# Optimization experiments

Measured on AMD Instinct MI355X. Metric: run time of the kernel, lower is better.

Reference implementation:

```python
import jax, jax.numpy as jnp
import numpy as np

H = 16  # n_heads

def setup_inputs() -> dict:
    key = jax.random.key(0)
    ks = jax.random.split(key, 8)
    B, S, D = 2, 2048, 1024
    q = jax.random.normal(ks[0], (B, S, D), dtype=jnp.float32)
    k = jax.random.normal(ks[1], (B, S, D), dtype=jnp.float32)
    v = jax.random.normal(ks[2], (B, S, D), dtype=jnp.float32)
    mask = jnp.ones((B, S, S), dtype=jnp.int32)
    scale = 1.0 / np.sqrt(D)
    Wq = jax.random.normal(ks[3], (D, D), dtype=jnp.float32) * scale
    Wk = jax.random.normal(ks[4], (D, D), dtype=jnp.float32) * scale
    Wv = jax.random.normal(ks[5], (D, D), dtype=jnp.float32) * scale
    Wo = jax.random.normal(ks[6], (D, D), dtype=jnp.float32) * scale
    return {"q": q, "k": k, "v": v, "mask": mask,
            "Wq": Wq, "Wk": Wk, "Wv": Wv, "Wo": Wo}

def reference(q, k, v, mask, Wq, Wk, Wv, Wo):
    B, S, D = q.shape
    dk = D // H
    # nn.Linear(bias=False): y = x @ W.T
    query = (q @ Wq.T).reshape(B, S, H, dk).transpose(0, 2, 1, 3)  # [B,H,S,dk]
    key_  = (k @ Wk.T).reshape(B, S, H, dk).transpose(0, 2, 1, 3)
    value = (v @ Wv.T).reshape(B, S, H, dk).transpose(0, 2, 1, 3)
    scores = jnp.einsum('bhqd,bhkd->bhqk', query, key_) / jnp.sqrt(jnp.float32(dk))
    scores = jnp.where(mask[:, None, :, :] == 0, jnp.float32(-1e9), scores)
    attn = jax.nn.softmax(scores, axis=-1)  # dropout=0.0 -> identity
    x = jnp.einsum('bhqk,bhkd->bhqd', attn, value)  # [B,H,S,dk]
    x = x.transpose(0, 2, 1, 3).reshape(B, S, D)
    return x @ Wo.T
```

## Files before the change

kernel.cpp:

```cpp
#include <hip/hip_runtime.h>
#include <hip/hip_bf16.h>

#define B_ 2
#define S_ 2048
#define D_ 1024
#define H_ 16

typedef __bf16 bf16x8 __attribute__((ext_vector_type(8)));
typedef __bf16 bf16x4v __attribute__((ext_vector_type(4)));
typedef float f32x4 __attribute__((ext_vector_type(4)));

__device__ __forceinline__ float exp2fast(float x) {
  return __builtin_amdgcn_exp2f(x);
}

__device__ __forceinline__ unsigned short f2bf(float f) {
  unsigned int u = __float_as_uint(f);
  u += 0x7fff + ((u >> 16) & 1);
  return (unsigned short)(u >> 16);
}

__device__ __forceinline__ void gload_lds16(const void* g, void* l) {
  __builtin_amdgcn_global_load_lds(
      (const __attribute__((address_space(1))) void*)g,
      (__attribute__((address_space(3))) void*)l, 16, 0, 0);
}

__global__ __launch_bounds__(256) void cvt_qkv(
    const float* __restrict__ a, const float* __restrict__ b, const float* __restrict__ c,
    unsigned short* __restrict__ da, unsigned short* __restrict__ db,
    unsigned short* __restrict__ dc, int n4) {
  const int z = blockIdx.z;
  const float* s = z == 0 ? a : (z == 1 ? b : c);
  unsigned short* d = z == 0 ? da : (z == 1 ? db : dc);
  int stride = gridDim.x * blockDim.x;
  for (int i = blockIdx.x * blockDim.x + threadIdx.x; i < n4; i += stride) {
    float4 f = ((const float4*)s)[i];
    ushort4 o;
    o.x = f2bf(f.x); o.y = f2bf(f.y); o.z = f2bf(f.z); o.w = f2bf(f.w);
    ((ushort4*)d)[i] = o;
  }
}

__global__ __launch_bounds__(256) void cvt_w(
    const float* __restrict__ a, const float* __restrict__ b,
    const float* __restrict__ c, const float* __restrict__ d,
    unsigned short* __restrict__ da, unsigned short* __restrict__ db,
    unsigned short* __restrict__ dc, unsigned short* __restrict__ dd, int n4) {
  const int z = blockIdx.z;
  const float* s = z == 0 ? a : (z == 1 ? b : (z == 2 ? c : d));
  unsigned short* o = z == 0 ? da : (z == 1 ? db : (z == 2 ? dc : dd));
  int stride = gridDim.x * blockDim.x;
  for (int i = blockIdx.x * blockDim.x + threadIdx.x; i < n4; i += stride) {
    float4 f = ((const float4*)s)[i];
    ushort4 u;
    u.x = f2bf(f.x); u.y = f2bf(f.y); u.z = f2bf(f.z); u.w = f2bf(f.w);
    ((ushort4*)o)[i] = u;
  }
}

__global__ __launch_bounds__(256) void mask_check(const int* __restrict__ m,
                                                  int* __restrict__ flag, int n4) {
  int stride = gridDim.x * blockDim.x;
  bool z = false;
  for (int i = blockIdx.x * blockDim.x + threadIdx.x; i < n4; i += stride) {
    int4 v = ((const int4*)m)[i];
    z |= (v.x == 0) || (v.y == 0) || (v.z == 0) || (v.w == 0);
  }
  if (__any(z)) {
    if ((threadIdx.x & 63) == 0) atomicOr(flag, 1);
  }
}

__device__ __forceinline__ void gemm_core(
    const unsigned short* __restrict__ A, const unsigned short* __restrict__ W,
    unsigned short* As, unsigned short* Bs, int rowBase, int colBase,
    f32x4 (&acc)[4][4]) {
  const int tid = threadIdx.x, lane = tid & 63, w = tid >> 6;
  const int wm = w >> 1, wn = w & 1, l15 = lane & 15, l4 = lane >> 4;
  for (int kt = 0; kt < 16; ++kt) {
#pragma unroll
    for (int i = 0; i < 4; i++) {
      int chunk = (w * 4 + i) * 64 + lane;
      int row = chunk >> 3, c = chunk & 7;
      int cs = c ^ (row & 7);
      gload_lds16(A + (size_t)(rowBase + row) * 1024 + kt * 64 + cs * 8,
                  (char*)As + (w * 4 + i) * 1024);
      gload_lds16(W + (size_t)(colBase + row) * 1024 + kt * 64 + cs * 8,
                  (char*)Bs + (w * 4 + i) * 1024);
    }
    __syncthreads();
#pragma unroll
    for (int ks = 0; ks < 2; ks++) {
      bf16x8 af[4], bfr[4];
#pragma unroll
      for (int mi = 0; mi < 4; mi++) {
        int row = wm * 64 + mi * 16 + l15;
        af[mi] = *(const bf16x8*)((const char*)As + row * 128 +
                                  (((ks * 4 + l4) ^ (row & 7)) << 4));
      }
#pragma unroll
      for (int ni = 0; ni < 4; ni++) {
        int row = wn * 64 + ni * 16 + l15;
        bfr[ni] = *(const bf16x8*)((const char*)Bs + row * 128 +
                                   (((ks * 4 + l4) ^ (row & 7)) << 4));
      }
#pragma unroll
      for (int mi = 0; mi < 4; mi++)
#pragma unroll
        for (int ni = 0; ni < 4; ni++)
          acc[mi][ni] = __builtin_amdgcn_mfma_f32_16x16x32_bf16(
              af[mi], bfr[ni], acc[mi][ni], 0, 0, 0);
    }
    __syncthreads();
  }
}

__global__ __launch_bounds__(256, 2) void gemm_qkv(
    const unsigned short* __restrict__ qA, const unsigned short* __restrict__ kA,
    const unsigned short* __restrict__ vA,
    const unsigned short* __restrict__ Wq, const unsigned short* __restrict__ Wk,
    const unsigned short* __restrict__ Wv,
    unsigned short* __restrict__ Qp, unsigned short* __restrict__ Kp,
    unsigned short* __restrict__ Vtp) {
  __shared__ unsigned short As[128 * 64], Bs[128 * 64];
  const int z = blockIdx.z;
  const unsigned short* A = z == 0 ? qA : (z == 1 ? kA : vA);
  const unsigned short* W = z == 0 ? Wq : (z == 1 ? Wk : Wv);
  const int rowBase = blockIdx.y * 128, colBase = blockIdx.x * 128;
  f32x4 acc[4][4] = {};
  gemm_core(A, W, As, Bs, rowBase, colBase, acc);
  const int tid = threadIdx.x, lane = tid & 63, w = tid >> 6;
  const int wm = w >> 1, wn = w & 1, l15 = lane & 15, l4 = lane >> 4;
#pragma unroll
  for (int mi = 0; mi < 4; mi++)
#pragma unroll
    for (int ni = 0; ni < 4; ni++)
#pragma unroll
      for (int r = 0; r < 4; r++) {
        int gr = rowBase + wm * 64 + mi * 16 + l4 * 4 + r;
        int gc = colBase + wn * 64 + ni * 16 + l15;
        int b = gr >> 11, s = gr & 2047, h = gc >> 6, d = gc & 63;
        float v = acc[mi][ni][r];
        if (z == 0)
          Qp[(((size_t)(b * 16 + h) * 2048 + s) << 6) + d] =
              f2bf(v * 0.18033688011112042f);
        else if (z == 1)
          Kp[(((size_t)(b * 16 + h) * 2048 + s) << 6) + d] = f2bf(v);
        else
          Vtp[((size_t)(b * 16 + h) * 64 + d) * 2048 + s] = f2bf(v);
      }
}

__global__ __launch_bounds__(256, 2) void gemm_o(
    const unsigned short* __restrict__ A, const unsigned short* __restrict__ W,
    float* __restrict__ Out) {
  __shared__ unsigned short As[128 * 64], Bs[128 * 64];
  const int rowBase = blockIdx.y * 128, colBase = blockIdx.x * 128;
  f32x4 acc[4][4] = {};
  gemm_core(A, W, As, Bs, rowBase, colBase, acc);
  const int tid = threadIdx.x, lane = tid & 63, w = tid >> 6;
  const int wm = w >> 1, wn = w & 1, l15 = lane & 15, l4 = lane >> 4;
#pragma unroll
  for (int mi = 0; mi < 4; mi++)
#pragma unroll
    for (int ni = 0; ni < 4; ni++)
#pragma unroll
      for (int r = 0; r < 4; r++) {
        int gr = rowBase + wm * 64 + mi * 16 + l4 * 4 + r;
        int gc = colBase + wn * 64 + ni * 16 + l15;
        Out[(size_t)gr * 1024 + gc] = acc[mi][ni][r];
      }
}

__global__ __launch_bounds__(256, 2) void attn(
    const unsigned short* __restrict__ Qp, const unsigned short* __restrict__ Kp,
    const unsigned short* __restrict__ Vt, unsigned short* __restrict__ Xo,
    const int* __restrict__ flag, const int* __restrict__ mask) {
  __shared__ unsigned short Ks[2][64 * 64];
  __shared__ unsigned short Vs[2][64 * 64];
  __shared__ unsigned short Pl[4][32][72];
  const int tid = threadIdx.x, lane = tid & 63, w = tid >> 6;
  const int l15 = lane & 15, l4 = lane >> 4;
  const int h = blockIdx.y, b = blockIdx.z;
  const int bh = b * H_ + h;
  const int q0 = blockIdx.x * 128 + w * 32;
  const int hz = *flag;

  bf16x8 qf[2][2];
#pragma unroll
  for (int qg = 0; qg < 2; qg++)
#pragma unroll
    for (int ks = 0; ks < 2; ks++)
      qf[qg][ks] = *(const bf16x8*)(Qp + ((size_t)bh * S_ + q0 + qg * 16 + l15) * 64 +
                                    ks * 32 + l4 * 8);

  float m[2] = {-__builtin_inff(), -__builtin_inff()};
  float l[2] = {0.f, 0.f};
  f32x4 accOT[2][4] = {};

  auto stage = [&](int kt, int buf) {
#pragma unroll
    for (int i = 0; i < 2; i++) {
      int ch = (w * 2 + i) * 64 + lane;
      int row = ch >> 3, c = ch & 7;
      int cs = c ^ (row & 7);
      gload_lds16(Kp + ((size_t)bh * S_ + kt * 64 + row) * 64 + cs * 8,
                  (char*)&Ks[buf][0] + (w * 2 + i) * 1024);
      gload_lds16(Vt + ((size_t)bh * 64 + row) * S_ + kt * 64 + cs * 8,
                  (char*)&Vs[buf][0] + (w * 2 + i) * 1024);
    }
  };

  stage(0, 0);
  __syncthreads();

  for (int kt = 0; kt < 32; ++kt) {
    const int cur = kt & 1;
    if (kt < 31) stage(kt + 1, cur ^ 1);

    f32x4 s[2][4] = {};
#pragma unroll
    for (int ks = 0; ks < 2; ks++) {
      bf16x8 kf[4];
#pragma unroll
      for (int kb = 0; kb < 4; kb++) {
        int row = kb * 16 + l15;
        kf[kb] = *(const bf16x8*)((const char*)&Ks[cur][0] + row * 128 +
                                  (((ks * 4 + l4) ^ (row & 7)) << 4));
      }
#pragma unroll
      for (int qg = 0; qg < 2; qg++)
#pragma unroll
        for (int kb = 0; kb < 4; kb++)
          s[qg][kb] = __builtin_amdgcn_mfma_f32_16x16x32_bf16(kf[kb], qf[qg][ks],
                                                              s[qg][kb], 0, 0, 0);
    }

    if (hz) {
#pragma unroll
      for (int qg = 0; qg < 2; qg++)
#pragma unroll
        for (int kb = 0; kb < 4; kb++)
#pragma unroll
          for (int r = 0; r < 4; r++) {
            int kc = kt * 64 + kb * 16 + l4 * 4 + r;
            if (mask[((size_t)b * S_ + q0 + qg * 16 + l15) * S_ + kc] == 0)
              s[qg][kb][r] = -1e9f;
          }
    }

    float mx[2];
#pragma unroll
    for (int qg = 0; qg < 2; qg++) {
      float m0 = fmaxf(fmaxf(s[qg][0][0], s[qg][0][1]), fmaxf(s[qg][0][2], s[qg][0][3]));
      float m1 = fmaxf(fmaxf(s[qg][1][0], s[qg][1][1]), fmaxf(s[qg][1][2], s[qg][1][3]));
      float m2 = fmaxf(fmaxf(s[qg][2][0], s[qg][2][1]), fmaxf(s[qg][2][2], s[qg][2][3]));
      float m3 = fmaxf(fmaxf(s[qg][3][0], s[qg][3][1]), fmaxf(s[qg][3][2], s[qg][3][3]));
      float v = fmaxf(fmaxf(m0, m1), fmaxf(m2, m3));
      v = fmaxf(v, __shfl_xor(v, 16));
      v = fmaxf(v, __shfl_xor(v, 32));
      mx[qg] = v;
    }

    if (!__all(mx[0] - m[0] <= 8.f && mx[1] - m[1] <= 8.f)) {
#pragma unroll
      for (int qg = 0; qg < 2; qg++) {
        float mn = fmaxf(m[qg], mx[qg]);
        float al = exp2fast(m[qg] - mn);
        m[qg] = mn;
        l[qg] *= al;
#pragma unroll
        for (int db = 0; db < 4; db++) accOT[qg][db] *= al;
      }
    }

#pragma unroll
    for (int qg = 0; qg < 2; qg++) {
      float rs = 0.f;
#pragma unroll
      for (int kb = 0; kb < 4; kb++) {
        bf16x4v pk;
#pragma unroll
        for (int r = 0; r < 4; r++) {
          float p = exp2fast(s[qg][kb][r] - m[qg]);
          rs += p;
          pk[r] = (__bf16)p;
        }
        *(bf16x4v*)(&Pl[w][qg * 16 + l15][kb * 16 + l4 * 4]) = pk;
      }
      rs += __shfl_xor(rs, 16);
      rs += __shfl_xor(rs, 32);
      l[qg] += rs;
    }

#pragma unroll
    for (int ks = 0; ks < 2; ks++) {
      bf16x8 vf[4], pa[2];
#pragma unroll
      for (int qg = 0; qg < 2; qg++)
        pa[qg] = *(const bf16x8*)((const char*)&Pl[w][qg * 16 + l15][0] +
                                  ks * 64 + l4 * 16);
#pragma unroll
      for (int db = 0; db < 4; db++) {
        int row = db * 16 + l15;
        vf[db] = *(const bf16x8*)((const char*)&Vs[cur][0] + row * 128 +
                                  (((ks * 4 + l4) ^ (row & 7)) << 4));
      }
#pragma unroll
      for (int qg = 0; qg < 2; qg++)
#pragma unroll
        for (int db = 0; db < 4; db++)
          accOT[qg][db] = __builtin_amdgcn_mfma_f32_16x16x32_bf16(vf[db], pa[qg],
                                                                  accOT[qg][db], 0, 0, 0);
    }
    __syncthreads();
  }

#pragma unroll
  for (int qg = 0; qg < 2; qg++) {
    float rl = 1.0f / l[qg];
    const int q = q0 + qg * 16 + l15;
#pragma unroll
    for (int db = 0; db < 4; db++) {
      bf16x4v o;
#pragma unroll
      for (int r = 0; r < 4; r++) o[r] = (__bf16)(accOT[qg][db][r] * rl);
      *(bf16x4v*)(Xo + (((size_t)(b * S_ + q)) << 10) + h * 64 + db * 16 + l4 * 4) = o;
    }
  }
}

extern "C" void kernel_launch(void* const* d_in, const int* in_sizes, int n_in,
                              void* d_out, int out_size, void* d_ws, size_t ws_size,
                              hipStream_t stream) {
  const float* q = (const float*)d_in[0];
  const float* k = (const float*)d_in[1];
  const float* v = (const float*)d_in[2];
  const int* mask = (const int*)d_in[3];
  const float* Wq = (const float*)d_in[4];
  const float* Wk = (const float*)d_in[5];
  const float* Wv = (const float*)d_in[6];
  const float* Wo = (const float*)d_in[7];

  char* ws = (char*)d_ws;
  const size_t MB = 1024 * 1024;
  unsigned short* qb16 = (unsigned short*)(ws);
  unsigned short* kb16 = (unsigned short*)(ws + 8 * MB);
  unsigned short* vb16 = (unsigned short*)(ws + 16 * MB);
  unsigned short* Wq16 = (unsigned short*)(ws + 24 * MB);
  unsigned short* Wk16 = (unsigned short*)(ws + 26 * MB);
  unsigned short* Wv16 = (unsigned short*)(ws + 28 * MB);
  unsigned short* Wo16 = (unsigned short*)(ws + 30 * MB);
  unsigned short* Qp = (unsigned short*)(ws + 32 * MB);
  unsigned short* Kp = (unsigned short*)(ws + 40 * MB);
  unsigned short* Vtp = (unsigned short*)(ws + 48 * MB);
  int* flag = (int*)(ws + 56 * MB);
  unsigned short* Xo = qb16;

  (void)hipMemsetAsync(flag, 0, 4, stream);
  cvt_qkv<<<dim3(1024, 1, 3), 256, 0, stream>>>(q, k, v, qb16, kb16, vb16,
                                                (B_ * S_ * D_) / 4);
  cvt_w<<<dim3(256, 1, 4), 256, 0, stream>>>(Wq, Wk, Wv, Wo, Wq16, Wk16, Wv16, Wo16,
                                             (D_ * D_) / 4);
  mask_check<<<dim3(2048), 256, 0, stream>>>(mask, flag, (B_ * S_ * S_) / 4);
  gemm_qkv<<<dim3(8, 32, 3), 256, 0, stream>>>(qb16, kb16, vb16, Wq16, Wk16, Wv16,
                                               Qp, Kp, Vtp);
  attn<<<dim3(16, 16, 2), 256, 0, stream>>>(Qp, Kp, Vtp, Xo, flag, mask);
  gemm_o<<<dim3(8, 32), 256, 0, stream>>>(Xo, Wo16, (float*)d_out);
}
```

Before: 158.3 us.

## Fuse prep kernels and load attention K/V directly into registers

The three conversion and mask-check kernels are merged into one prep launch, which removes launch overhead and lets the launches overlap. The attention kernel drops its LDS staging and block-wide barriers for K and V: each wave loads K and V fragments straight from global memory into registers, with K double-buffered in registers. The attention grid is also remapped so blocks that share a head are spread across the grid. In exchange, every wave re-reads the same K/V tiles from global memory or L2, and register pressure goes up.

New measurement: 208.0 us. 1.31x slower.

```diff
diff --git a/kernel.cpp b/kernel.cpp
--- a/kernel.cpp
+++ b/kernel.cpp
@@ -26,49 +26,53 @@
       (__attribute__((address_space(3))) void*)l, 16, 0, 0);
 }
 
-__global__ __launch_bounds__(256) void cvt_qkv(
-    const float* __restrict__ a, const float* __restrict__ b, const float* __restrict__ c,
-    unsigned short* __restrict__ da, unsigned short* __restrict__ db,
-    unsigned short* __restrict__ dc, int n4) {
+__global__ __launch_bounds__(256) void prep(
+    const float* __restrict__ q, const float* __restrict__ k,
+    const float* __restrict__ v, const int* __restrict__ mask,
+    const float* __restrict__ Wq, const float* __restrict__ Wk,
+    const float* __restrict__ Wv, const float* __restrict__ Wo,
+    unsigned short* __restrict__ qb, unsigned short* __restrict__ kb,
+    unsigned short* __restrict__ vb,
+    unsigned short* __restrict__ Wqb, unsigned short* __restrict__ Wkb,
+    unsigned short* __restrict__ Wvb, unsigned short* __restrict__ Wob,
+    int* __restrict__ flag) {
   const int z = blockIdx.z;
-  const float* s = z == 0 ? a : (z == 1 ? b : c);
-  unsigned short* d = z == 0 ? da : (z == 1 ? db : dc);
-  int stride = gridDim.x * blockDim.x;
-  for (int i = blockIdx.x * blockDim.x + threadIdx.x; i < n4; i += stride) {
-    float4 f = ((const float4*)s)[i];
-    ushort4 o;
-    o.x = f2bf(f.x); o.y = f2bf(f.y); o.z = f2bf(f.z); o.w = f2bf(f.w);
-    ((ushort4*)d)[i] = o;
-  }
-}
-
-__global__ __launch_bounds__(256) void cvt_w(
-    const float* __restrict__ a, const float* __restrict__ b,
-    const float* __restrict__ c, const float* __restrict__ d,
-    unsigned short* __restrict__ da, unsigned short* __restrict__ db,
-    unsigned short* __restrict__ dc, unsigned short* __restrict__ dd, int n4) {
-  const int z = blockIdx.z;
-  const float* s = z == 0 ? a : (z == 1 ? b : (z == 2 ? c : d));
-  unsigned short* o = z == 0 ? da : (z == 1 ? db : (z == 2 ? dc : dd));
-  int stride = gridDim.x * blockDim.x;
-  for (int i = blockIdx.x * blockDim.x + threadIdx.x; i < n4; i += stride) {
-    float4 f = ((const float4*)s)[i];
-    ushort4 u;
-    u.x = f2bf(f.x); u.y = f2bf(f.y); u.z = f2bf(f.z); u.w = f2bf(f.w);
-    ((ushort4*)o)[i] = u;
-  }
-}
-
-__global__ __launch_bounds__(256) void mask_check(const int* __restrict__ m,
-                                                  int* __restrict__ flag, int n4) {
-  int stride = gridDim.x * blockDim.x;
-  bool z = false;
-  for (int i = blockIdx.x * blockDim.x + threadIdx.x; i < n4; i += stride) {
-    int4 v = ((const int4*)m)[i];
-    z |= (v.x == 0) || (v.y == 0) || (v.z == 0) || (v.w == 0);
-  }
-  if (__any(z)) {
-    if ((threadIdx.x & 63) == 0) atomicOr(flag, 1);
+  const int stride = gridDim.x * blockDim.x;
+  const int tid0 = blockIdx.x * blockDim.x + threadIdx.x;
+  if (z < 3) {
+    const float* s = z == 0 ? q : (z == 1 ? k : v);
+    unsigned short* d = z == 0 ? qb : (z == 1 ? kb : vb);
+    const int n4 = B_ * S_ * D_ / 4;
+    for (int i = tid0; i < n4; i += stride) {
+      float4 f = ((const float4*)s)[i];
+      ushort4 o;
+      o.x = f2bf(f.x); o.y = f2bf(f.y); o.z = f2bf(f.z); o.w = f2bf(f.w);
+      ((ushort4*)d)[i] = o;
+    }
+  } else if (z == 3) {
+    const int n4 = D_ * D_ / 4;
+#pragma unroll
+    for (int t = 0; t < 4; t++) {
+      const float* s = t == 0 ? Wq : (t == 1 ? Wk : (t == 2 ? Wv : Wo));
+      unsigned short* d = t == 0 ? Wqb : (t == 1 ? Wkb : (t == 2 ? Wvb : Wob));
+      for (int i = tid0; i < n4; i += stride) {
+        float4 f = ((const float4*)s)[i];
+        ushort4 o;
+        o.x = f2bf(f.x); o.y = f2bf(f.y); o.z = f2bf(f.z); o.w = f2bf(f.w);
+        ((ushort4*)d)[i] = o;
+      }
+    }
+  } else {
+    const int half = B_ * S_ * S_ / 8;
+    const int base = (z - 4) * half;
+    bool zf = false;
+    for (int i = tid0; i < half; i += stride) {
+      int4 mv = ((const int4*)mask)[base + i];
+      zf |= (mv.x == 0) || (mv.y == 0) || (mv.z == 0) || (mv.w == 0);
+    }
+    if (__any(zf)) {
+      if ((threadIdx.x & 63) == 0) atomicOr(flag, 1);
+    }
   }
 }
 
@@ -177,15 +181,19 @@
     const unsigned short* __restrict__ Qp, const unsigned short* __restrict__ Kp,
     const unsigned short* __restrict__ Vt, unsigned short* __restrict__ Xo,
     const int* __restrict__ flag, const int* __restrict__ mask) {
-  __shared__ unsigned short Ks[2][64 * 64];
-  __shared__ unsigned short Vs[2][64 * 64];
   __shared__ unsigned short Pl[4][32][72];
   const int tid = threadIdx.x, lane = tid & 63, w = tid >> 6;
   const int l15 = lane & 15, l4 = lane >> 4;
-  const int h = blockIdx.y, b = blockIdx.z;
-  const int bh = b * H_ + h;
-  const int q0 = blockIdx.x * 128 + w * 32;
+
+  const int bid = ((blockIdx.x & 7) << 6) + (blockIdx.x >> 3);
+  const int qblk = bid & 15;
+  const int bh = bid >> 4;
+  const int h = bh & 15, b = bh >> 4;
+  const int q0 = qblk * 128 + w * 32;
   const int hz = *flag;
+
+  const unsigned short* Kbase = Kp + (size_t)bh * S_ * 64;
+  const unsigned short* Vbase = Vt + (size_t)bh * 64 * S_;
 
   bf16x8 qf[2][2];
 #pragma unroll
@@ -199,43 +207,37 @@
   float l[2] = {0.f, 0.f};
   f32x4 accOT[2][4] = {};
 
-  auto stage = [&](int kt, int buf) {
-#pragma unroll
-    for (int i = 0; i < 2; i++) {
-      int ch = (w * 2 + i) * 64 + lane;
-      int row = ch >> 3, c = ch & 7;
-      int cs = c ^ (row & 7);
-      gload_lds16(Kp + ((size_t)bh * S_ + kt * 64 + row) * 64 + cs * 8,
-                  (char*)&Ks[buf][0] + (w * 2 + i) * 1024);
-      gload_lds16(Vt + ((size_t)bh * 64 + row) * S_ + kt * 64 + cs * 8,
-                  (char*)&Vs[buf][0] + (w * 2 + i) * 1024);
-    }
+  auto loadK = [&](int kt, bf16x8 (&kf)[2][4]) {
+#pragma unroll
+    for (int ks = 0; ks < 2; ks++)
+#pragma unroll
+      for (int kb = 0; kb < 4; kb++)
+        kf[ks][kb] = *(const bf16x8*)(Kbase + (size_t)(kt * 64 + kb * 16 + l15) * 64 +
+                                      ks * 32 + l4 * 8);
   };
-
-  stage(0, 0);
-  __syncthreads();
-
-  for (int kt = 0; kt < 32; ++kt) {
-    const int cur = kt & 1;
-    if (kt < 31) stage(kt + 1, cur ^ 1);
+  auto loadV = [&](int kt, bf16x8 (&vf)[2][4]) {
+#pragma unroll
+    for (int ks = 0; ks < 2; ks++)
+#pragma unroll
+      for (int db = 0; db < 4; db++)
+        vf[ks][db] = *(const bf16x8*)(Vbase + (size_t)(db * 16 + l15) * S_ +
+                                      kt * 64 + ks * 32 + l4 * 8);
+  };
+
+  auto step = [&](int kt, bf16x8 (&kfC)[2][4], bf16x8 (&kfN)[2][4]) {
+    bf16x8 vf[2][4];
+    loadV(kt, vf);
+    if (kt + 1 < 32) loadK(kt + 1, kfN);
 
     f32x4 s[2][4] = {};
 #pragma unroll
-    for (int ks = 0; ks < 2; ks++) {
-      bf16x8 kf[4];
-#pragma unroll
-      for (int kb = 0; kb < 4; kb++) {
-        int row = kb * 16 + l15;
-        kf[kb] = *(const bf16x8*)((const char*)&Ks[cur][0] + row * 128 +
-                                  (((ks * 4 + l4) ^ (row & 7)) << 4));
-      }
+    for (int ks = 0; ks < 2; ks++)
 #pragma unroll
       for (int qg = 0; qg < 2; qg++)
 #pragma unroll
         for (int kb = 0; kb < 4; kb++)
-          s[qg][kb] = __builtin_amdgcn_mfma_f32_16x16x32_bf16(kf[kb], qf[qg][ks],
+          s[qg][kb] = __builtin_amdgcn_mfma_f32_16x16x32_bf16(kfC[ks][kb], qf[qg][ks],
                                                               s[qg][kb], 0, 0, 0);
-    }
 
     if (hz) {
 #pragma unroll
@@ -296,25 +298,25 @@
 
 #pragma unroll
     for (int ks = 0; ks < 2; ks++) {
-      bf16x8 vf[4], pa[2];
+      bf16x8 pa[2];
 #pragma unroll
       for (int qg = 0; qg < 2; qg++)
         pa[qg] = *(const bf16x8*)((const char*)&Pl[w][qg * 16 + l15][0] +
                                   ks * 64 + l4 * 16);
 #pragma unroll
-      for (int db = 0; db < 4; db++) {
-        int row = db * 16 + l15;
-        vf[db] = *(const bf16x8*)((const char*)&Vs[cur][0] + row * 128 +
-                                  (((ks * 4 + l4) ^ (row & 7)) << 4));
-      }
-#pragma unroll
       for (int qg = 0; qg < 2; qg++)
 #pragma unroll
         for (int db = 0; db < 4; db++)
-          accOT[qg][db] = __builtin_amdgcn_mfma_f32_16x16x32_bf16(vf[db], pa[qg],
+          accOT[qg][db] = __builtin_amdgcn_mfma_f32_16x16x32_bf16(vf[ks][db], pa[qg],
                                                                   accOT[qg][db], 0, 0, 0);
     }
-    __syncthreads();
+  };
+
+  bf16x8 kfA[2][4], kfB[2][4];
+  loadK(0, kfA);
+  for (int kt = 0; kt < 32; kt += 2) {
+    step(kt, kfA, kfB);
+    step(kt + 1, kfB, kfA);
   }
 
 #pragma unroll
@@ -359,13 +361,11 @@
   unsigned short* Xo = qb16;
 
   (void)hipMemsetAsync(flag, 0, 4, stream);
-  cvt_qkv<<<dim3(1024, 1, 3), 256, 0, stream>>>(q, k, v, qb16, kb16, vb16,
-                                                (B_ * S_ * D_) / 4);
-  cvt_w<<<dim3(256, 1, 4), 256, 0, stream>>>(Wq, Wk, Wv, Wo, Wq16, Wk16, Wv16, Wo16,
-                                             (D_ * D_) / 4);
-  mask_check<<<dim3(2048), 256, 0, stream>>>(mask, flag, (B_ * S_ * S_) / 4);
+  prep<<<dim3(1024, 1, 6), 256, 0, stream>>>(q, k, v, mask, Wq, Wk, Wv, Wo,
+                                             qb16, kb16, vb16, Wq16, Wk16, Wv16,
+                                             Wo16, flag);
   gemm_qkv<<<dim3(8, 32, 3), 256, 0, stream>>>(qb16, kb16, vb16, Wq16, Wk16, Wv16,
                                                Qp, Kp, Vtp);
-  attn<<<dim3(16, 16, 2), 256, 0, stream>>>(Qp, Kp, Vtp, Xo, flag, mask);
+  attn<<<dim3(512), 256, 0, stream>>>(Qp, Kp, Vtp, Xo, flag, mask);
   gemm_o<<<dim3(8, 32), 256, 0, stream>>>(Xo, Wo16, (float*)d_out);
 }
```
